# Performance work log

Hardware: AMD Instinct MI355X
Metric: run time of the kernel (lower is better)

## Reference

```python
import jax, jax.numpy as jnp
import numpy as np

C_IN = 128
C_HID = 128


def setup_inputs() -> dict:
    key = jax.random.key(0)
    ks = jax.random.split(key, 10)
    B, I, J = 1, 384, 384
    x = jax.random.normal(ks[0], (B, I, J, C_IN), dtype=jnp.float32)
    mask = jnp.ones((B, I, J), dtype=jnp.float32)
    # LayerNorm params
    ln_gamma = jnp.ones((C_IN,), jnp.float32)
    ln_beta = jnp.zeros((C_IN,), jnp.float32)
    # Projections (stored as [in, out] for x @ W)
    W_a_p = jax.random.normal(ks[1], (C_IN, C_HID), jnp.float32) * 0.02
    b_a_p = jnp.zeros((C_HID,), jnp.float32)
    W_a_g = jax.random.normal(ks[2], (C_IN, C_HID), jnp.float32) * 0.01
    W_b_p = jax.random.normal(ks[3], (C_IN, C_HID), jnp.float32) * 0.02
    b_b_p = jnp.zeros((C_HID,), jnp.float32)
    W_b_g = jax.random.normal(ks[4], (C_IN, C_HID), jnp.float32) * 0.01
    W_z = jax.random.normal(ks[5], (C_HID, C_IN), jnp.float32) * (0.02 / np.sqrt(C_HID))
    b_z = jnp.zeros((C_IN,), jnp.float32)
    return dict(x=x, mask=mask, ln_gamma=ln_gamma, ln_beta=ln_beta,
                W_a_p=W_a_p, b_a_p=b_a_p, W_a_g=W_a_g,
                W_b_p=W_b_p, b_b_p=b_b_p, W_b_g=W_b_g,
                W_z=W_z, b_z=b_z)


def _layer_norm(x, gamma, beta, eps=1e-5):
    mu = jnp.mean(x, axis=-1, keepdims=True)
    var = jnp.mean(jnp.square(x - mu), axis=-1, keepdims=True)
    return (x - mu) * jax.lax.rsqrt(var + eps) * gamma + beta


def reference(x, mask, ln_gamma, ln_beta, W_a_p, b_a_p, W_a_g, W_b_p, b_b_p, W_b_g, W_z, b_z):
    # x: [B, I, J, C_in], mask: [B, I, J]; outgoing triangle multiplication
    xn = _layer_norm(x, ln_gamma, ln_beta)
    m = mask[..., None]
    a = (xn @ W_a_p + b_a_p) * jax.nn.sigmoid(xn @ W_a_g) * m  # [B,I,J,Ch]
    b = (xn @ W_b_p + b_b_p) * jax.nn.sigmoid(xn @ W_b_g) * m  # [B,I,J,Ch]
    # outgoing: sum over k of a[...,i,k,c] * b[...,k,j,c]
    o = jnp.einsum('bikc,bkjc->bijc', a, b)
    o = o @ W_z + b_z
    return x + o
```

## Files before the change

kernel.cpp:

```cpp
#include <hip/hip_runtime.h>

typedef __bf16 bf16;
typedef bf16 bf16x4 __attribute__((ext_vector_type(4)));
typedef bf16 bf16x8 __attribute__((ext_vector_type(8)));
typedef float f32x4 __attribute__((ext_vector_type(4)));
typedef int ivec4 __attribute__((ext_vector_type(4)));

#define PTOT 147456
#define N384 384

static __device__ __forceinline__ f32x4 mfma16(bf16x8 a, bf16x8 b, f32x4 c) {
  return __builtin_amdgcn_mfma_f32_16x16x32_bf16(a, b, c, 0, 0, 0);
}

static __device__ __forceinline__ void gload_lds16(const bf16* g, bf16* lds) {
  __builtin_amdgcn_global_load_lds(
      (const __attribute__((address_space(1))) void*)g,
      (__attribute__((address_space(3))) void*)lds, 16, 0, 0);
}

__global__ __launch_bounds__(256) void k_prep(
    const float* __restrict__ w0, const float* __restrict__ w1,
    const float* __restrict__ w2, const float* __restrict__ w3,
    const float* __restrict__ w4, bf16* __restrict__ wt)
{
  const int m = blockIdx.x;
  const float* src = (m == 0) ? w0 : (m == 1) ? w1 : (m == 2) ? w2 : (m == 3) ? w3 : w4;
  for (int slot = threadIdx.x; slot < 2048; slot += 256) {
    const int l  = slot & 63;
    const int ks = (slot >> 6) & 3;
    const int n  = slot >> 8;
    const int ch = n * 16 + (l & 15);
    const int kb = ks * 32 + (l >> 4) * 8;
    bf16 tmp[8] __attribute__((aligned(16)));
    #pragma unroll
    for (int e = 0; e < 8; ++e)
      tmp[e] = (bf16)src[(size_t)(kb + e) * 128 + ch];
    bf16* dst = (m < 4)
        ? wt + (size_t)((n * 16 + m * 4 + ks) * 64 + l) * 8
        : wt + 4 * 16384 + (size_t)((n * 4 + ks) * 64 + l) * 8;
    *(ivec4*)dst = *(const ivec4*)tmp;
  }
}

__global__ __launch_bounds__(512, 4) void k1_ln_proj(
    const float* __restrict__ x, const float* __restrict__ mask,
    const float* __restrict__ gamma, const float* __restrict__ beta,
    const float* __restrict__ bap, const float* __restrict__ bbp,
    const bf16* __restrict__ wt,
    bf16* __restrict__ a_t, bf16* __restrict__ b_t)
{
  __shared__ __align__(16) bf16 xn[128 * 128];
  __shared__ __align__(16) bf16 wl[2 * 8192];
  __shared__ float ml[128];

  const int t = threadIdx.x;
  const int l = t & 63;
  const int w = t >> 6;
  const int p0 = blockIdx.x << 7;
  const int fr = l & 15, fq = l >> 4;
  const int pair = w & 1;
  const int prow0 = (w >> 1) * 32;

  const bf16* wsrc = wt + l * 8;
  const int c0 = w * 2;
  gload_lds16(wsrc + ((c0) << 9),     wl + c0 * 512);
  gload_lds16(wsrc + ((c0 + 1) << 9), wl + (c0 + 1) * 512);

  if (t < 128) ml[t] = mask[p0 + t];

  const int csub = (t & 7) << 4;
  f32x4 g4[4], bt4[4];
  #pragma unroll
  for (int i = 0; i < 4; ++i) {
    g4[i]  = *(const f32x4*)(gamma + csub + i * 4);
    bt4[i] = *(const f32x4*)(beta  + csub + i * 4);
  }
  #pragma unroll
  for (int it = 0; it < 2; ++it) {
    const int row = (t >> 3) + it * 64;
    f32x4 v[4];
    const float* xb = x + (size_t)(p0 + row) * 128 + csub;
    #pragma unroll
    for (int i = 0; i < 4; ++i) v[i] = *(const f32x4*)(xb + i * 4);

    float s = 0.f, s2 = 0.f;
    #pragma unroll
    for (int i = 0; i < 4; ++i)
      #pragma unroll
      for (int j = 0; j < 4; ++j) { const float f = v[i][j]; s += f; s2 += f * f; }
    #pragma unroll
    for (int m = 1; m < 8; m <<= 1) {
      s  += __shfl_xor(s, m, 64);
      s2 += __shfl_xor(s2, m, 64);
    }
    const float mu = s * (1.f / 128.f);
    const float rs = rsqrtf(s2 * (1.f / 128.f) - mu * mu + 1e-5f);

    bf16x8 xv0, xv1;
    #pragma unroll
    for (int i = 0; i < 4; ++i)
      #pragma unroll
      for (int j = 0; j < 4; ++j) {
        const float f = (v[i][j] - mu) * rs * g4[i][j] + bt4[i][j];
        const int e = i * 4 + j;
        if (e < 8) xv0[e] = (bf16)f; else xv1[e - 8] = (bf16)f;
      }
    const int sw = (row & 7) << 3;
    *(bf16x8*)&xn[row * 128 + (csub ^ sw)]       = xv0;
    *(bf16x8*)&xn[row * 128 + ((csub + 8) ^ sw)] = xv1;
  }
  __syncthreads();

  bf16x8 af[2][4];
  #pragma unroll
  for (int mi = 0; mi < 2; ++mi)
    #pragma unroll
    for (int ks = 0; ks < 4; ++ks) {
      const int row = prow0 + mi * 16 + fr;
      af[mi][ks] = *(const bf16x8*)&xn[row * 128 + ((ks * 32 + fq * 8) ^ ((fr & 7) << 3))];
    }

  const float* bp = pair ? bbp : bap;
  bf16* dst = pair ? b_t : a_t;
  float biasv[8];
  #pragma unroll
  for (int p = 0; p < 8; ++p) biasv[p] = bp[p * 16 + fr];

  #pragma unroll
  for (int p = 0; p < 8; ++p) {
    if (p < 7) {
      bf16* nb = wl + ((p + 1) & 1) * 8192;
      gload_lds16(wsrc + (((p + 1) * 16 + c0) << 9),     nb + c0 * 512);
      gload_lds16(wsrc + (((p + 1) * 16 + c0 + 1) << 9), nb + (c0 + 1) * 512);
    }
    const bf16* buf = wl + (p & 1) * 8192 + l * 8;
    const bf16* wpl = buf + (pair * 2) * 2048;
    const bf16* wgl = buf + (pair * 2 + 1) * 2048;

    f32x4 aG0 = (f32x4){0.f, 0.f, 0.f, 0.f};
    f32x4 aG1 = (f32x4){0.f, 0.f, 0.f, 0.f};
    #pragma unroll
    for (int ks = 0; ks < 4; ++ks) {
      const bf16x8 bv = *(const bf16x8*)(wgl + ks * 512);
      aG0 = mfma16(af[0][ks], bv, aG0);
      aG1 = mfma16(af[1][ks], bv, aG1);
    }
    f32x4 aP0 = (f32x4){0.f, 0.f, 0.f, 0.f};
    f32x4 aP1 = (f32x4){0.f, 0.f, 0.f, 0.f};
    #pragma unroll
    for (int ks = 0; ks < 4; ++ks) {
      const bf16x8 bv = *(const bf16x8*)(wpl + ks * 512);
      aP0 = mfma16(af[0][ks], bv, aP0);
      aP1 = mfma16(af[1][ks], bv, aP1);
    }
    const int ch = p * 16 + fr;
    const float bias = biasv[p];
    #pragma unroll
    for (int mi = 0; mi < 2; ++mi) {
      const f32x4 aG = mi ? aG1 : aG0;
      const f32x4 aP = mi ? aP1 : aP0;
      const int pb = prow0 + mi * 16 + fq * 4;
      const f32x4 m4 = *(const f32x4*)&ml[pb];
      bf16x4 pk;
      #pragma unroll
      for (int r = 0; r < 4; ++r) {
        const float sg = 1.f / (1.f + __expf(-aG[r]));
        pk[r] = (bf16)((aP[r] + bias) * sg * m4[r]);
      }
      *(bf16x4*)(dst + (size_t)ch * PTOT + p0 + pb) = pk;
    }
    if (p < 7) __syncthreads();
  }
}

__global__ __launch_bounds__(256) void k2_tri(
    const bf16* __restrict__ a_t, const bf16* __restrict__ b_t, bf16* __restrict__ o_t)
{
  __shared__ __align__(16) bf16 As[128][40];
  __shared__ __align__(16) bf16 Bt[128][40];
  const int t = threadIdx.x, l = t & 63, w = t >> 6;
  const int fr = l & 15, fq = l >> 4;
  const int ti = blockIdx.x;
  const int c  = blockIdx.y;
  const int i0 = (ti / 3) * 128, j0 = (ti % 3) * 128;
  const bf16* ap = a_t + (size_t)c * PTOT;
  const bf16* bp = b_t + (size_t)c * PTOT;
  const int wm = (w >> 1) * 64, wn = (w & 1) * 64;
  const int arow = t >> 2, aseg = t & 3;
  const int bj = t & 127, bkh = (t >> 7) * 16;

  f32x4 acc[4][4];
  #pragma unroll
  for (int mi = 0; mi < 4; ++mi)
    #pragma unroll
    for (int ni = 0; ni < 4; ++ni) acc[mi][ni] = (f32x4){0.f, 0.f, 0.f, 0.f};

  for (int kt = 0; kt < 12; ++kt) {
    const int k0 = kt * 32;
    __syncthreads();
    #pragma unroll
    for (int rep = 0; rep < 2; ++rep) {
      const int row = arow + rep * 64;
      *(ivec4*)&As[row][aseg * 8] =
          *(const ivec4*)(ap + (size_t)(i0 + row) * N384 + k0 + aseg * 8);
    }
    bf16 rb[16] __attribute__((aligned(16)));
    #pragma unroll
    for (int kk = 0; kk < 16; ++kk)
      rb[kk] = bp[(size_t)(k0 + bkh + kk) * N384 + j0 + bj];
    *(ivec4*)&Bt[bj][bkh]     = *(const ivec4*)&rb[0];
    *(ivec4*)&Bt[bj][bkh + 8] = *(const ivec4*)&rb[8];
    __syncthreads();

    bf16x8 af[4], bfv[4];
    #pragma unroll
    for (int mi = 0; mi < 4; ++mi)
      af[mi] = *(const bf16x8*)&As[wm + mi * 16 + fr][fq * 8];
    #pragma unroll
    for (int ni = 0; ni < 4; ++ni)
      bfv[ni] = *(const bf16x8*)&Bt[wn + ni * 16 + fr][fq * 8];
    #pragma unroll
    for (int mi = 0; mi < 4; ++mi)
      #pragma unroll
      for (int ni = 0; ni < 4; ++ni)
        acc[mi][ni] = mfma16(bfv[ni], af[mi], acc[mi][ni]);
  }

  bf16* op = o_t + (size_t)c * PTOT;
  #pragma unroll
  for (int mi = 0; mi < 4; ++mi) {
    const int irow = i0 + wm + mi * 16 + fr;
    #pragma unroll
    for (int ni = 0; ni < 4; ++ni) {
      const int jcol = j0 + wn + ni * 16 + fq * 4;
      bf16x4 pk;
      #pragma unroll
      for (int r = 0; r < 4; ++r) pk[r] = (bf16)acc[mi][ni][r];
      *(bf16x4*)(op + (size_t)irow * N384 + jcol) = pk;
    }
  }
}

__global__ __launch_bounds__(256) void k3_out(
    const bf16* __restrict__ o_t, const bf16* __restrict__ wtz,
    const float* __restrict__ x, const float* __restrict__ bz,
    float* __restrict__ out)
{
  __shared__ __align__(16) bf16 Ao[64][136];
  const int t = threadIdx.x, l = t & 63, w = t >> 6;
  const int fr = l & 15, fq = l >> 4;
  const int p0 = blockIdx.x << 6;
  const int pos = t & 63, chh = (t >> 6) * 32;

  bf16 rb[32] __attribute__((aligned(16)));
  #pragma unroll
  for (int cc = 0; cc < 32; ++cc)
    rb[cc] = o_t[(size_t)(chh + cc) * PTOT + p0 + pos];
  #pragma unroll
  for (int q = 0; q < 4; ++q)
    *(ivec4*)&Ao[pos][chh + q * 8] = *(const ivec4*)&rb[q * 8];
  __syncthreads();

  bf16x8 af[4];
  #pragma unroll
  for (int ks = 0; ks < 4; ++ks)
    af[ks] = *(const bf16x8*)&Ao[w * 16 + fr][ks * 32 + fq * 8];

  const bf16* wzf = wtz + l * 8;
  f32x4 acc[8];
  #pragma unroll
  for (int n = 0; n < 8; ++n) acc[n] = (f32x4){0.f, 0.f, 0.f, 0.f};
  #pragma unroll
  for (int n = 0; n < 8; ++n)
    #pragma unroll
    for (int ks = 0; ks < 4; ++ks) {
      const bf16x8 bfv = *(const bf16x8*)(wzf + ((n * 4 + ks) << 9));
      acc[n] = mfma16(bfv, af[ks], acc[n]);
    }

  const int pp = p0 + w * 16 + fr;
  #pragma unroll
  for (int n = 0; n < 8; ++n) {
    const int ch = n * 16 + fq * 4;
    const f32x4 b4 = *(const f32x4*)(bz + ch);
    const size_t idx = (size_t)pp * 128 + ch;
    const f32x4 x4 = *(const f32x4*)(x + idx);
    f32x4 o4;
    #pragma unroll
    for (int r = 0; r < 4; ++r) o4[r] = x4[r] + acc[n][r] + b4[r];
    *(f32x4*)(out + idx) = o4;
  }
}

extern "C" void kernel_launch(void* const* d_in, const int* in_sizes, int n_in,
                              void* d_out, int out_size, void* d_ws, size_t ws_size,
                              hipStream_t stream) {
  const float* x     = (const float*)d_in[0];
  const float* mask  = (const float*)d_in[1];
  const float* gamma = (const float*)d_in[2];
  const float* beta  = (const float*)d_in[3];
  const float* Wap   = (const float*)d_in[4];
  const float* bap   = (const float*)d_in[5];
  const float* Wag   = (const float*)d_in[6];
  const float* Wbp   = (const float*)d_in[7];
  const float* bbp   = (const float*)d_in[8];
  const float* Wbg   = (const float*)d_in[9];
  const float* Wz    = (const float*)d_in[10];
  const float* bz    = (const float*)d_in[11];

  char* ws = (char*)d_ws;
  bf16* wt  = (bf16*)ws;
  bf16* a_t = (bf16*)(ws + 163840);
  bf16* b_t = a_t + (size_t)128 * PTOT;
  bf16* o_t = b_t + (size_t)128 * PTOT;
  float* out = (float*)d_out;

  k_prep<<<5, 256, 0, stream>>>(Wap, Wag, Wbp, Wbg, Wz, wt);
  k1_ln_proj<<<1152, 512, 0, stream>>>(x, mask, gamma, beta, bap, bbp, wt, a_t, b_t);
  k2_tri<<<dim3(9, 128), 256, 0, stream>>>(a_t, b_t, o_t);
  k3_out<<<2304, 256, 0, stream>>>(o_t, wt + 4 * 16384, x, bz, out);
}
```

Baseline: 143.9 us.

## Double-buffer k2 tiles with vectorized B loads, swizzle LDS, resize k1 and k_prep grids

The triangle GEMM kernel now double-buffers its A and B tiles in swizzled LDS. B is read with 16-byte vector loads, and pairs of k rows are packed into 32-bit LDS writes in place of strided scalar gathers, with global loads for the next k-tile issued before the MFMAs. The output projection kernel likewise replaces 32 scalar strided loads per thread with vector loads and a swizzled LDS transpose. k1 drops to 256 threads per block with 64 positions per block and twice as many blocks, and k_prep spreads over 40 blocks. Together these aim to raise memory coalescing, hide load latency and improve occupancy and parallelism, at the cost of extra LDS write instructions and register pressure.

```diff
diff --git a/kernel.cpp b/kernel.cpp
--- a/kernel.cpp
+++ b/kernel.cpp
@@ -24,50 +24,48 @@
     const float* __restrict__ w2, const float* __restrict__ w3,
     const float* __restrict__ w4, bf16* __restrict__ wt)
 {
-  const int m = blockIdx.x;
+  const int m = blockIdx.x >> 3, n = blockIdx.x & 7;
   const float* src = (m == 0) ? w0 : (m == 1) ? w1 : (m == 2) ? w2 : (m == 3) ? w3 : w4;
-  for (int slot = threadIdx.x; slot < 2048; slot += 256) {
-    const int l  = slot & 63;
-    const int ks = (slot >> 6) & 3;
-    const int n  = slot >> 8;
-    const int ch = n * 16 + (l & 15);
-    const int kb = ks * 32 + (l >> 4) * 8;
-    bf16 tmp[8] __attribute__((aligned(16)));
-    #pragma unroll
-    for (int e = 0; e < 8; ++e)
-      tmp[e] = (bf16)src[(size_t)(kb + e) * 128 + ch];
-    bf16* dst = (m < 4)
-        ? wt + (size_t)((n * 16 + m * 4 + ks) * 64 + l) * 8
-        : wt + 4 * 16384 + (size_t)((n * 4 + ks) * 64 + l) * 8;
-    *(ivec4*)dst = *(const ivec4*)tmp;
-  }
-}
-
-__global__ __launch_bounds__(512, 4) void k1_ln_proj(
+  const int t = threadIdx.x;
+  const int ks = t >> 6, l = t & 63;
+  const int ch = n * 16 + (l & 15);
+  const int kb = ks * 32 + (l >> 4) * 8;
+  bf16 tmp[8] __attribute__((aligned(16)));
+  #pragma unroll
+  for (int e = 0; e < 8; ++e)
+    tmp[e] = (bf16)src[(size_t)(kb + e) * 128 + ch];
+  bf16* dst = (m < 4)
+      ? wt + (size_t)((n * 16 + m * 4 + ks) * 64 + l) * 8
+      : wt + 4 * 16384 + (size_t)((n * 4 + ks) * 64 + l) * 8;
+  *(ivec4*)dst = *(const ivec4*)tmp;
+}
+
+__global__ __launch_bounds__(256) void k1_ln_proj(
     const float* __restrict__ x, const float* __restrict__ mask,
     const float* __restrict__ gamma, const float* __restrict__ beta,
     const float* __restrict__ bap, const float* __restrict__ bbp,
     const bf16* __restrict__ wt,
     bf16* __restrict__ a_t, bf16* __restrict__ b_t)
 {
-  __shared__ __align__(16) bf16 xn[128 * 128];
+  __shared__ __align__(16) bf16 xn[64 * 128];
   __shared__ __align__(16) bf16 wl[2 * 8192];
-  __shared__ float ml[128];
+  __shared__ float ml[64];
 
   const int t = threadIdx.x;
   const int l = t & 63;
   const int w = t >> 6;
-  const int p0 = blockIdx.x << 7;
+  const int p0 = blockIdx.x << 6;
   const int fr = l & 15, fq = l >> 4;
   const int pair = w & 1;
   const int prow0 = (w >> 1) * 32;
 
   const bf16* wsrc = wt + l * 8;
-  const int c0 = w * 2;
-  gload_lds16(wsrc + ((c0) << 9),     wl + c0 * 512);
-  gload_lds16(wsrc + ((c0 + 1) << 9), wl + (c0 + 1) * 512);
-
-  if (t < 128) ml[t] = mask[p0 + t];
+  const int c0 = w * 4;
+  #pragma unroll
+  for (int j = 0; j < 4; ++j)
+    gload_lds16(wsrc + ((c0 + j) << 9), wl + (c0 + j) * 512);
+
+  if (t < 64) ml[t] = mask[p0 + t];
 
   const int csub = (t & 7) << 4;
   f32x4 g4[4], bt4[4];
@@ -78,7 +76,7 @@
   }
   #pragma unroll
   for (int it = 0; it < 2; ++it) {
-    const int row = (t >> 3) + it * 64;
+    const int row = (t >> 3) + it * 32;
     f32x4 v[4];
     const float* xb = x + (size_t)(p0 + row) * 128 + csub;
     #pragma unroll
@@ -131,8 +129,9 @@
   for (int p = 0; p < 8; ++p) {
     if (p < 7) {
       bf16* nb = wl + ((p + 1) & 1) * 8192;
-      gload_lds16(wsrc + (((p + 1) * 16 + c0) << 9),     nb + c0 * 512);
-      gload_lds16(wsrc + (((p + 1) * 16 + c0 + 1) << 9), nb + (c0 + 1) * 512);
+      #pragma unroll
+      for (int j = 0; j < 4; ++j)
+        gload_lds16(wsrc + (((p + 1) * 16 + c0 + j) << 9), nb + (c0 + j) * 512);
     }
     const bf16* buf = wl + (p & 1) * 8192 + l * 8;
     const bf16* wpl = buf + (pair * 2) * 2048;
@@ -177,8 +176,8 @@
 __global__ __launch_bounds__(256) void k2_tri(
     const bf16* __restrict__ a_t, const bf16* __restrict__ b_t, bf16* __restrict__ o_t)
 {
-  __shared__ __align__(16) bf16 As[128][40];
-  __shared__ __align__(16) bf16 Bt[128][40];
+  __shared__ __align__(16) bf16 As[2][4096];
+  __shared__ __align__(16) bf16 Bs[2][4096];
   const int t = threadIdx.x, l = t & 63, w = t >> 6;
   const int fr = l & 15, fq = l >> 4;
   const int ti = blockIdx.x;
@@ -188,7 +187,8 @@
   const bf16* bp = b_t + (size_t)c * PTOT;
   const int wm = (w >> 1) * 64, wn = (w & 1) * 64;
   const int arow = t >> 2, aseg = t & 3;
-  const int bj = t & 127, bkh = (t >> 7) * 16;
+  const int asw = (aseg ^ ((arow >> 3) & 3)) << 3;
+  const int qb = t >> 4, jb = (t & 15) * 8;
 
   f32x4 acc[4][4];
   #pragma unroll
@@ -196,35 +196,63 @@
     #pragma unroll
     for (int ni = 0; ni < 4; ++ni) acc[mi][ni] = (f32x4){0.f, 0.f, 0.f, 0.f};
 
+  ivec4 ga0, ga1, gb0, gb1;
+  ga0 = *(const ivec4*)(ap + (size_t)(i0 + arow) * N384 + aseg * 8);
+  ga1 = *(const ivec4*)(ap + (size_t)(i0 + arow + 64) * N384 + aseg * 8);
+  gb0 = *(const ivec4*)(bp + (size_t)(2 * qb) * N384 + j0 + jb);
+  gb1 = *(const ivec4*)(bp + (size_t)(2 * qb + 1) * N384 + j0 + jb);
+  {
+    *(ivec4*)&As[0][arow * 32 + asw] = ga0;
+    *(ivec4*)&As[0][(arow + 64) * 32 + asw] = ga1;
+    union { ivec4 v; unsigned short u[8]; } ua, ub;
+    ua.v = gb0; ub.v = gb1;
+    #pragma unroll
+    for (int e = 0; e < 8; ++e) {
+      const int j = jb + e;
+      const unsigned int pk = (unsigned int)ua.u[e] | ((unsigned int)ub.u[e] << 16);
+      *(unsigned int*)&Bs[0][j * 32 + (((qb >> 2) ^ ((j >> 3) & 3)) << 3) + ((qb & 3) << 1)] = pk;
+    }
+  }
+
   for (int kt = 0; kt < 12; ++kt) {
-    const int k0 = kt * 32;
     __syncthreads();
-    #pragma unroll
-    for (int rep = 0; rep < 2; ++rep) {
-      const int row = arow + rep * 64;
-      *(ivec4*)&As[row][aseg * 8] =
-          *(const ivec4*)(ap + (size_t)(i0 + row) * N384 + k0 + aseg * 8);
-    }
-    bf16 rb[16] __attribute__((aligned(16)));
-    #pragma unroll
-    for (int kk = 0; kk < 16; ++kk)
-      rb[kk] = bp[(size_t)(k0 + bkh + kk) * N384 + j0 + bj];
-    *(ivec4*)&Bt[bj][bkh]     = *(const ivec4*)&rb[0];
-    *(ivec4*)&Bt[bj][bkh + 8] = *(const ivec4*)&rb[8];
-    __syncthreads();
-
+    const int cur = kt & 1;
     bf16x8 af[4], bfv[4];
     #pragma unroll
-    for (int mi = 0; mi < 4; ++mi)
-      af[mi] = *(const bf16x8*)&As[wm + mi * 16 + fr][fq * 8];
-    #pragma unroll
-    for (int ni = 0; ni < 4; ++ni)
-      bfv[ni] = *(const bf16x8*)&Bt[wn + ni * 16 + fr][fq * 8];
+    for (int mi = 0; mi < 4; ++mi) {
+      const int row = wm + mi * 16 + fr;
+      af[mi] = *(const bf16x8*)&As[cur][row * 32 + ((fq ^ ((row >> 3) & 3)) << 3)];
+    }
+    #pragma unroll
+    for (int ni = 0; ni < 4; ++ni) {
+      const int j = wn + ni * 16 + fr;
+      bfv[ni] = *(const bf16x8*)&Bs[cur][j * 32 + ((fq ^ ((j >> 3) & 3)) << 3)];
+    }
+    if (kt < 11) {
+      const int k0 = (kt + 1) * 32;
+      ga0 = *(const ivec4*)(ap + (size_t)(i0 + arow) * N384 + k0 + aseg * 8);
+      ga1 = *(const ivec4*)(ap + (size_t)(i0 + arow + 64) * N384 + k0 + aseg * 8);
+      gb0 = *(const ivec4*)(bp + (size_t)(k0 + 2 * qb) * N384 + j0 + jb);
+      gb1 = *(const ivec4*)(bp + (size_t)(k0 + 2 * qb + 1) * N384 + j0 + jb);
+    }
     #pragma unroll
     for (int mi = 0; mi < 4; ++mi)
       #pragma unroll
       for (int ni = 0; ni < 4; ++ni)
         acc[mi][ni] = mfma16(bfv[ni], af[mi], acc[mi][ni]);
+    if (kt < 11) {
+      const int nxt = cur ^ 1;
+      *(ivec4*)&As[nxt][arow * 32 + asw] = ga0;
+      *(ivec4*)&As[nxt][(arow + 64) * 32 + asw] = ga1;
+      union { ivec4 v; unsigned short u[8]; } ua, ub;
+      ua.v = gb0; ub.v = gb1;
+      #pragma unroll
+      for (int e = 0; e < 8; ++e) {
+        const int j = jb + e;
+        const unsigned int pk = (unsigned int)ua.u[e] | ((unsigned int)ub.u[e] << 16);
+        *(unsigned int*)&Bs[nxt][j * 32 + (((qb >> 2) ^ ((j >> 3) & 3)) << 3) + ((qb & 3) << 1)] = pk;
+      }
+    }
   }
 
   bf16* op = o_t + (size_t)c * PTOT;
@@ -247,25 +275,34 @@
     const float* __restrict__ x, const float* __restrict__ bz,
     float* __restrict__ out)
 {
-  __shared__ __align__(16) bf16 Ao[64][136];
+  __shared__ __align__(16) bf16 Ao[64 * 128];
   const int t = threadIdx.x, l = t & 63, w = t >> 6;
   const int fr = l & 15, fq = l >> 4;
   const int p0 = blockIdx.x << 6;
-  const int pos = t & 63, chh = (t >> 6) * 32;
-
-  bf16 rb[32] __attribute__((aligned(16)));
-  #pragma unroll
-  for (int cc = 0; cc < 32; ++cc)
-    rb[cc] = o_t[(size_t)(chh + cc) * PTOT + p0 + pos];
-  #pragma unroll
-  for (int q = 0; q < 4; ++q)
-    *(ivec4*)&Ao[pos][chh + q * 8] = *(const ivec4*)&rb[q * 8];
+  const int ps = t & 7, cb = t >> 3;
+
+  #pragma unroll
+  for (int rep = 0; rep < 2; ++rep) {
+    const int cc = cb + 32 * rep;
+    ivec4 d0 = *(const ivec4*)(o_t + (size_t)(2 * cc) * PTOT + p0 + ps * 8);
+    ivec4 d1 = *(const ivec4*)(o_t + (size_t)(2 * cc + 1) * PTOT + p0 + ps * 8);
+    union { ivec4 v; unsigned short u[8]; } ua, ub;
+    ua.v = d0; ub.v = d1;
+    #pragma unroll
+    for (int e = 0; e < 8; ++e) {
+      const int p = ps * 8 + e;
+      const unsigned int pk = (unsigned int)ua.u[e] | ((unsigned int)ub.u[e] << 16);
+      *(unsigned int*)&Ao[p * 128 + (((cc >> 2) ^ (p & 15)) << 3) + ((cc & 3) << 1)] = pk;
+    }
+  }
   __syncthreads();
 
   bf16x8 af[4];
   #pragma unroll
-  for (int ks = 0; ks < 4; ++ks)
-    af[ks] = *(const bf16x8*)&Ao[w * 16 + fr][ks * 32 + fq * 8];
+  for (int ks = 0; ks < 4; ++ks) {
+    const int p = w * 16 + fr;
+    af[ks] = *(const bf16x8*)&Ao[p * 128 + (((ks * 4 + fq) ^ fr) << 3)];
+  }
 
   const bf16* wzf = wtz + l * 8;
   f32x4 acc[8];
@@ -316,8 +353,8 @@
   bf16* o_t = b_t + (size_t)128 * PTOT;
   float* out = (float*)d_out;
 
-  k_prep<<<5, 256, 0, stream>>>(Wap, Wag, Wbp, Wbg, Wz, wt);
-  k1_ln_proj<<<1152, 512, 0, stream>>>(x, mask, gamma, beta, bap, bbp, wt, a_t, b_t);
+  k_prep<<<40, 256, 0, stream>>>(Wap, Wag, Wbp, Wbg, Wz, wt);
+  k1_ln_proj<<<2304, 256, 0, stream>>>(x, mask, gamma, beta, bap, bbp, wt, a_t, b_t);
   k2_tri<<<dim3(9, 128), 256, 0, stream>>>(a_t, b_t, o_t);
   k3_out<<<2304, 256, 0, stream>>>(o_t, wt + 4 * 16384, x, bz, out);
 }
```

Result: no change. 143.9 us (-0.0%).
